# Optimization experiments

Measured on AMD Instinct MI355X. Metric: run time of the kernel, lower is better.

Reference implementation:

```python
import jax, jax.numpy as jnp
import numpy as np

N, C_IN, C_OUT, K, S, P, H, W = 16, 64, 128, 3, 1, 1, 224, 224

def setup_inputs() -> dict:
    key = jax.random.key(0)
    kx, kw = jax.random.split(key)
    x = jax.random.normal(kx, (N, C_IN, H, W), dtype=jnp.float32)
    weight = jax.random.normal(kw, (C_OUT, C_IN, K, K), dtype=jnp.float32)
    bias = jnp.zeros((C_OUT,), dtype=jnp.float32)
    return {"x": x, "weight": weight, "bias": bias}

def reference(x, weight, bias):
    # im2col + matmul with stride 1 is exactly a standard conv2d with SAME-style padding P
    out = jax.lax.conv_general_dilated(
        x, weight,
        window_strides=(S, S),
        padding=((P, P), (P, P)),
        dimension_numbers=("NCHW", "OIHW", "NCHW"),
    )
    return out + bias[None, :, None, None]  # [N, C_OUT, H, W]
```

## Files before the change

kernel.cpp:

```cpp
#include <hip/hip_runtime.h>
#include <cstdint>
#include <cstddef>


typedef short bf16x8 __attribute__((ext_vector_type(8)));
typedef float f32x4 __attribute__((ext_vector_type(4)));

#define N_ 16
#define CI_ 64
#define CO_ 128
#define H_ 224
#define W_ 224
#define HW_ (H_ * W_)

#define WP_ 226
#define CBS_ 1808ULL
#define HPS_ 14464ULL
#define NS_ 3268864ULL

__device__ __forceinline__ unsigned short f2bf(float f) {
    unsigned u = __builtin_bit_cast(unsigned, f);
    u += 0x7FFFu + ((u >> 16) & 1u);
    return (unsigned short)(u >> 16);
}

__global__ void prep_weight(const float* __restrict__ w, unsigned short* __restrict__ wr) {
    int i = blockIdx.x * 256 + threadIdx.x;
    if (i >= 9 * CO_ * CI_) return;
    int ci = i & 63;
    int co = (i >> 6) & 127;
    int t  = i >> 13;
    wr[i] = f2bf(w[(co * CI_ + ci) * 9 + t]);
}

__global__ __launch_bounds__(256) void prep_x(const float* __restrict__ x,
                                              unsigned short* __restrict__ xp) {
    int b = blockIdx.x;
    int n = b / 226, hp = b - n * 226;
    int tid = threadIdx.x;
    unsigned short* row = xp + (size_t)n * NS_ + (size_t)hp * HPS_;
    if (hp == 0 || hp == 225) {
        #pragma unroll
        for (int k = 0; k < 8; ++k) {
            int i = k * 256 + tid;
            if (i < 1808) ((uint4*)row)[i] = make_uint4(0, 0, 0, 0);
        }
        return;
    }
    int h = hp - 1;
    const float* xb = x + (size_t)n * CI_ * HW_ + (size_t)h * W_;
    for (int k = 0; k < 7; ++k) {
        int item = k * 256 + tid;
        int w = item % 224;
        int cb = item / 224;
        unsigned r[4];
        #pragma unroll
        for (int c = 0; c < 4; ++c) {
            float lo = xb[(size_t)(cb * 8 + 2 * c) * HW_ + w];
            float hi = xb[(size_t)(cb * 8 + 2 * c + 1) * HW_ + w];
            r[c] = (unsigned)f2bf(lo) | ((unsigned)f2bf(hi) << 16);
        }
        *(uint4*)(row + (size_t)cb * CBS_ + (size_t)(w + 1) * 8) = make_uint4(r[0], r[1], r[2], r[3]);
    }
    if (tid < 16) {
        int cb = tid >> 1, wp = (tid & 1) * 225;
        *(uint4*)(row + (size_t)cb * CBS_ + (size_t)wp * 8) = make_uint4(0, 0, 0, 0);
    }
}

__global__ __launch_bounds__(256, 2) void conv2(
    const unsigned short* __restrict__ xp, const unsigned short* __restrict__ wr,
    const float* __restrict__ bias, float* __restrict__ out)
{
    __shared__ __align__(16) unsigned short xs[4 * 8 * 114 * 8];

    int bid = blockIdx.x;
    int swz = (bid & 7) * 448 + (bid >> 3);
    int n = swz / 224;
    int r2 = swz - n * 224;
    int hblk = r2 >> 1;
    int wseg = r2 & 1;
    int h0 = hblk * 2;

    int tid = threadIdx.x, lane = tid & 63, wid = tid >> 6;
    int hr = wid & 1, mh = wid >> 1;
    int lrow = lane & 15, lk = lane >> 4;

    f32x4 acc[4][7];
    #pragma unroll
    for (int a = 0; a < 4; ++a)
        #pragma unroll
        for (int b2 = 0; b2 < 7; ++b2)
            #pragma unroll
            for (int k = 0; k < 4; ++k)
                acc[a][b2][k] = 0.0f;

    const unsigned short* xpn = xp + (size_t)n * NS_;

    #pragma unroll
    for (int it = 0; it < 14; ++it) {
        int idx = it * 256 + tid;
        int wp = idx % 114;
        int rc = idx / 114;
        const unsigned short* src = xpn + (size_t)(h0 + (rc >> 3)) * HPS_
                                  + (size_t)(rc & 7) * CBS_ + (size_t)(wseg * 112 + wp) * 8;
        __builtin_amdgcn_global_load_lds(
            (const __attribute__((address_space(1))) void*)src,
            (__attribute__((address_space(3))) void*)(xs + (size_t)idx * 8),
            16, 0, 0);
    }
    if (tid < 64) {
        int idx = 3584 + tid;
        int wp = idx % 114;
        int rc = idx / 114;
        const unsigned short* src = xpn + (size_t)(h0 + (rc >> 3)) * HPS_
                                  + (size_t)(rc & 7) * CBS_ + (size_t)(wseg * 112 + wp) * 8;
        __builtin_amdgcn_global_load_lds(
            (const __attribute__((address_space(1))) void*)src,
            (__attribute__((address_space(3))) void*)(xs + (size_t)idx * 8),
            16, 0, 0);
    }
    __syncthreads();

    #pragma unroll
    for (int ch = 0; ch < 2; ++ch) {
        #pragma unroll
        for (int t = 0; t < 9; ++t) {
            int kh = t / 3, kw = t - kh * 3;
            bf16x8 afr[4];
            #pragma unroll
            for (int mf = 0; mf < 4; ++mf) {
                size_t ai = ((size_t)(t * 128 + mh * 64 + mf * 16 + lrow)) * 64
                          + (size_t)(ch * 32 + lk * 8);
                afr[mf] = *(const bf16x8*)(wr + ai);
            }
            int rbase = ((hr + kh) * 8 + ch * 4 + lk) * 114;
            int wpb = lrow + kw;
            #pragma unroll
            for (int nf = 0; nf < 7; ++nf) {
                bf16x8 bfr = *(const bf16x8*)(&xs[(size_t)(rbase + wpb + nf * 16) * 8]);
                #pragma unroll
                for (int mf = 0; mf < 4; ++mf)
                    acc[mf][nf] = __builtin_amdgcn_mfma_f32_16x16x32_bf16(
                        afr[mf], bfr, acc[mf][nf], 0, 0, 0);
            }
        }
    }

    __syncthreads();
    float* lf = (float*)xs;
    int h = h0 + hr;
    #pragma unroll
    for (int mf = 0; mf < 4; ++mf) {
        float bv[4];
        #pragma unroll
        for (int r = 0; r < 4; ++r)
            bv[r] = bias[mh * 64 + mf * 16 + lk * 4 + r];
        float* wbase = lf + wid * 1808 + lk * 452 + lrow;
        #pragma unroll
        for (int r = 0; r < 4; ++r)
            #pragma unroll
            for (int nf = 0; nf < 7; ++nf)
                wbase[r * 112 + nf * 16] = acc[mf][nf][r] + bv[r];
        #pragma unroll
        for (int j = 0; j < 7; ++j) {
            int idx4 = j * 64 + lane;
            int col = idx4 / 28;
            int w4  = idx4 - col * 28;
            f32x4 v = *(const f32x4*)(lf + wid * 1808 + (col >> 2) * 452 + (col & 3) * 112 + w4 * 4);
            size_t ob = (((size_t)n * CO_ + mh * 64 + mf * 16 + col) * H_ + h) * W_
                      + wseg * 112 + w4 * 4;
            *(f32x4*)(out + ob) = v;
        }
    }
}

__global__ __launch_bounds__(512, 2) void conv_mfma(
    const float* __restrict__ x, const unsigned short* __restrict__ wr,
    const float* __restrict__ bias, float* __restrict__ out)
{
    __shared__ unsigned short xs[4 * 4 * 226 * 8];
    int bid = blockIdx.x;
    int swz = (bid & 7) * 224 + (bid >> 3);
    int n = swz / 112;
    int hblk = swz - n * 112;
    int h0 = hblk * 2;
    int tid = threadIdx.x;
    int lane = tid & 63;
    int wid = tid >> 6;
    int hr = wid & 1, nh = (wid >> 1) & 1, mh = wid >> 2;
    int lrow = lane & 15, lk = lane >> 4;

    f32x4 acc[4][7];
    #pragma unroll
    for (int a = 0; a < 4; ++a)
        #pragma unroll
        for (int b = 0; b < 7; ++b)
            #pragma unroll
            for (int k = 0; k < 4; ++k)
                acc[a][b][k] = 0.0f;

    for (int ch = 0; ch < 2; ++ch) {
        if (ch) __syncthreads();
        const float* xb = x + ((size_t)n * CI_ + (size_t)ch * 32) * HW_;
        int wcol = tid % 224;
        int rem = tid / 224;
        for (int it = 0; it < 7; ++it) {
            float v[8]; int bi[8];
            #pragma unroll
            for (int u = 0; u < 8; ++u) {
                int ciL = rem & 31;
                int r4 = rem >> 5;
                int hh = h0 - 1 + r4;
                float val = 0.0f;
                if ((unsigned)hh < (unsigned)H_)
                    val = xb[(size_t)ciL * HW_ + (size_t)hh * W_ + wcol];
                v[u] = val;
                bi[u] = (((r4 << 2) + (ciL >> 3)) * 226 + wcol + 1) * 8 + (ciL & 7);
                wcol += 64; rem += 2;
                if (wcol >= 224) { wcol -= 224; rem += 1; }
            }
            #pragma unroll
            for (int u = 0; u < 8; ++u)
                xs[bi[u]] = f2bf(v[u]);
        }
        if (tid < 256) {
            int wp = (tid & 1) * 225;
            int ciL = (tid >> 1) & 31;
            int r4 = tid >> 6;
            xs[(((r4 << 2) + (ciL >> 3)) * 226 + wp) * 8 + (ciL & 7)] = 0;
        }
        __syncthreads();

        #pragma unroll
        for (int t = 0; t < 9; ++t) {
            int kh = t / 3, kw = t - kh * 3;
            bf16x8 afr[4];
            #pragma unroll
            for (int mf = 0; mf < 4; ++mf) {
                size_t ai = ((size_t)(t * 128 + mh * 64 + mf * 16 + lrow)) * 64
                          + (size_t)(ch * 32 + lk * 8);
                afr[mf] = *(const bf16x8*)(wr + ai);
            }
            int rbase = ((hr + kh) * 4 + lk) * 226;
            int wpb = nh * 112 + lrow + kw;
            #pragma unroll
            for (int nf = 0; nf < 7; ++nf) {
                bf16x8 bfr = *(const bf16x8*)(&xs[(size_t)(rbase + wpb + nf * 16) * 8]);
                #pragma unroll
                for (int mf = 0; mf < 4; ++mf)
                    acc[mf][nf] = __builtin_amdgcn_mfma_f32_16x16x32_bf16(
                        afr[mf], bfr, acc[mf][nf], 0, 0, 0);
            }
        }
    }

    int h = h0 + hr;
    #pragma unroll
    for (int mf = 0; mf < 4; ++mf) {
        #pragma unroll
        for (int r = 0; r < 4; ++r) {
            int co = mh * 64 + mf * 16 + lk * 4 + r;
            float bv = bias[co];
            size_t ob = (((size_t)n * CO_ + co) * H_ + h) * W_ + nh * 112 + lrow;
            #pragma unroll
            for (int nf = 0; nf < 7; ++nf)
                out[ob + (size_t)nf * 16] = acc[mf][nf][r] + bv;
        }
    }
}

extern "C" void kernel_launch(void* const* d_in, const int* in_sizes, int n_in,
                              void* d_out, int out_size, void* d_ws, size_t ws_size,
                              hipStream_t stream) {
    const float* x    = (const float*)d_in[0];
    const float* w    = (const float*)d_in[1];
    const float* bias = (const float*)d_in[2];
    float* out = (float*)d_out;
    unsigned short* wr = (unsigned short*)d_ws;
    const size_t xp_bytes = (size_t)N_ * NS_ * 2;
    const size_t need = 147456 + xp_bytes;

    prep_weight<<<dim3(288), dim3(256), 0, stream>>>(w, wr);
    if (ws_size >= need) {
        unsigned short* xp = wr + 73728;
        prep_x<<<dim3(16 * 226), dim3(256), 0, stream>>>(x, xp);
        conv2<<<dim3(16 * 112 * 2), dim3(256), 0, stream>>>(xp, wr, bias, out);
    } else {
        conv_mfma<<<dim3(16 * 112), dim3(512), 0, stream>>>(x, wr, bias, out);
    }
}
```

Baseline: 286.5 us.

## Add row-streaming conv kernel with LDS ring buffer reusing input rows

```diff
diff --git a/kernel.cpp b/kernel.cpp
--- a/kernel.cpp
+++ b/kernel.cpp
@@ -17,6 +17,9 @@
 #define CBS_ 1808ULL
 #define HPS_ 14464ULL
 #define NS_ 3268864ULL
+
+#define ROWBUF_SHORTS 7296
+#define CONV3_LDS 145408
 
 __device__ __forceinline__ unsigned short f2bf(float f) {
     unsigned u = __builtin_bit_cast(unsigned, f);
@@ -65,6 +68,118 @@
     if (tid < 16) {
         int cb = tid >> 1, wp = (tid & 1) * 225;
         *(uint4*)(row + (size_t)cb * CBS_ + (size_t)wp * 8) = make_uint4(0, 0, 0, 0);
+    }
+}
+
+__global__ __launch_bounds__(512, 2) void conv3(
+    const unsigned short* __restrict__ xp, const unsigned short* __restrict__ wr,
+    const float* __restrict__ bias, float* __restrict__ out)
+{
+    extern __shared__ __align__(16) unsigned short ring[];
+    float* bounce = (float*)ring + 6 * ROWBUF_SHORTS / 2;
+
+    int bid = blockIdx.x;
+    int swz = (bid & 7) * 32 + (bid >> 3);
+    int n = swz >> 4;
+    int rem = swz & 15;
+    int wseg = rem & 1;
+    int strip = rem >> 1;
+    int ho0 = strip * 28;
+
+    int tid = threadIdx.x, lane = tid & 63, wid = tid >> 6;
+    int hr = wid & 1, mq = wid >> 1;
+    int lrow = lane & 15, lk = lane >> 4;
+
+    const unsigned short* xpn = xp + (size_t)n * NS_;
+
+    auto stage_row = [&](int hp) {
+        const unsigned short* srow = xpn + (size_t)hp * HPS_ + (size_t)(wseg * 112) * 8;
+        unsigned short* dbase = ring + (size_t)(hp % 6) * ROWBUF_SHORTS;
+        int idx = tid;
+        {
+            int cb = idx / 114, wp = idx - cb * 114;
+            __builtin_amdgcn_global_load_lds(
+                (const __attribute__((address_space(1))) void*)(srow + (size_t)cb * CBS_ + (size_t)wp * 8),
+                (__attribute__((address_space(3))) void*)(dbase + (size_t)idx * 8), 16, 0, 0);
+        }
+        idx = 512 + tid;
+        if (idx < 912) {
+            int cb = idx / 114, wp = idx - cb * 114;
+            __builtin_amdgcn_global_load_lds(
+                (const __attribute__((address_space(1))) void*)(srow + (size_t)cb * CBS_ + (size_t)wp * 8),
+                (__attribute__((address_space(3))) void*)(dbase + (size_t)idx * 8), 16, 0, 0);
+        }
+    };
+
+    stage_row(ho0); stage_row(ho0 + 1); stage_row(ho0 + 2); stage_row(ho0 + 3);
+    __syncthreads();
+
+    #pragma unroll 1
+    for (int i = 0; i < 14; ++i) {
+        int ho = ho0 + 2 * i;
+
+        if (i < 13) { stage_row(ho + 4); stage_row(ho + 5); }
+
+        f32x4 acc[2][7];
+        #pragma unroll
+        for (int a = 0; a < 2; ++a)
+            #pragma unroll
+            for (int b2 = 0; b2 < 7; ++b2)
+                #pragma unroll
+                for (int k = 0; k < 4; ++k)
+                    acc[a][b2][k] = 0.0f;
+
+        #pragma unroll
+        for (int ch = 0; ch < 2; ++ch) {
+            #pragma unroll
+            for (int t = 0; t < 9; ++t) {
+                int kh = t / 3, kw = t - kh * 3;
+                bf16x8 afr[2];
+                #pragma unroll
+                for (int mf = 0; mf < 2; ++mf) {
+                    size_t ai = ((size_t)(t * 128 + mq * 32 + mf * 16 + lrow)) * 64
+                              + (size_t)(ch * 32 + lk * 8);
+                    afr[mf] = *(const bf16x8*)(wr + ai);
+                }
+                int slot = (ho + hr + kh) % 6;
+                int rb = slot * ROWBUF_SHORTS + ((ch * 4 + lk) * 114) * 8;
+                int wb = lrow + kw;
+                #pragma unroll
+                for (int nf = 0; nf < 7; ++nf) {
+                    bf16x8 bfr = *(const bf16x8*)(ring + rb + (size_t)(wb + nf * 16) * 8);
+                    acc[0][nf] = __builtin_amdgcn_mfma_f32_16x16x32_bf16(afr[0], bfr, acc[0][nf], 0, 0, 0);
+                    acc[1][nf] = __builtin_amdgcn_mfma_f32_16x16x32_bf16(afr[1], bfr, acc[1][nf], 0, 0, 0);
+                }
+            }
+        }
+
+        float* lf = bounce + wid * 1808;
+        int h = ho + hr;
+        #pragma unroll
+        for (int mf = 0; mf < 2; ++mf) {
+            float bv[4];
+            #pragma unroll
+            for (int r = 0; r < 4; ++r)
+                bv[r] = bias[mq * 32 + mf * 16 + lk * 4 + r];
+            float* wbase = lf + lk * 452 + lrow;
+            #pragma unroll
+            for (int r = 0; r < 4; ++r)
+                #pragma unroll
+                for (int nf = 0; nf < 7; ++nf)
+                    wbase[r * 112 + nf * 16] = acc[mf][nf][r] + bv[r];
+            #pragma unroll
+            for (int j = 0; j < 7; ++j) {
+                int idx4 = j * 64 + lane;
+                int col = idx4 / 28;
+                int w4  = idx4 - col * 28;
+                f32x4 v = *(const f32x4*)(lf + (col >> 2) * 452 + (col & 3) * 112 + w4 * 4);
+                size_t ob = (((size_t)n * CO_ + mq * 32 + mf * 16 + col) * H_ + h) * W_
+                          + wseg * 112 + w4 * 4;
+                *(f32x4*)(out + ob) = v;
+            }
+        }
+
+        __syncthreads();
     }
 }
 
@@ -106,8 +221,7 @@
                                   + (size_t)(rc & 7) * CBS_ + (size_t)(wseg * 112 + wp) * 8;
         __builtin_amdgcn_global_load_lds(
             (const __attribute__((address_space(1))) void*)src,
-            (__attribute__((address_space(3))) void*)(xs + (size_t)idx * 8),
-            16, 0, 0);
+            (__attribute__((address_space(3))) void*)(xs + (size_t)idx * 8), 16, 0, 0);
     }
     if (tid < 64) {
         int idx = 3584 + tid;
@@ -117,8 +231,7 @@
                                   + (size_t)(rc & 7) * CBS_ + (size_t)(wseg * 112 + wp) * 8;
         __builtin_amdgcn_global_load_lds(
             (const __attribute__((address_space(1))) void*)src,
-            (__attribute__((address_space(3))) void*)(xs + (size_t)idx * 8),
-            16, 0, 0);
+            (__attribute__((address_space(3))) void*)(xs + (size_t)idx * 8), 16, 0, 0);
     }
     __syncthreads();
 
@@ -285,7 +398,14 @@
     if (ws_size >= need) {
         unsigned short* xp = wr + 73728;
         prep_x<<<dim3(16 * 226), dim3(256), 0, stream>>>(x, xp);
-        conv2<<<dim3(16 * 112 * 2), dim3(256), 0, stream>>>(xp, wr, bias, out);
+        hipError_t e = hipFuncSetAttribute(
+            reinterpret_cast<const void*>(conv3),
+            hipFuncAttributeMaxDynamicSharedMemorySize, CONV3_LDS);
+        if (e == hipSuccess) {
+            conv3<<<dim3(256), dim3(512), CONV3_LDS, stream>>>(xp, wr, bias, out);
+        } else {
+            conv2<<<dim3(16 * 112 * 2), dim3(256), 0, stream>>>(xp, wr, bias, out);
+        }
     } else {
         conv_mfma<<<dim3(16 * 112), dim3(512), 0, stream>>>(x, wr, bias, out);
     }
```

New measurement: 243.8 us. -14.9%, faster.
